# Optimization experiments

Measured on AMD Instinct MI355X. Metric: run time of the kernel, lower is better.

## Reference

```python
import jax, jax.numpy as jnp
import numpy as np

N_NODES = 100000
IN_CH = 65
HID_CH = 64
N_EDGES = 3200000


def setup_inputs() -> dict:
    key = jax.random.key(0)
    k1, k2, k3, k4, k5 = jax.random.split(key, 5)
    x = jax.random.normal(k1, (N_NODES, IN_CH), dtype=jnp.float32)
    edge_index = jax.random.randint(k2, (2, N_EDGES), 0, N_NODES, dtype=jnp.int64)
    edge_weight = jax.random.uniform(k3, (N_EDGES,), dtype=jnp.float32)
    # PyG GraphConv params: lin_rel (with bias) applied to aggregated neighbors,
    # lin_root (no bias) applied to self features.
    scale = 1.0 / np.sqrt(IN_CH)
    W_rel = jax.random.uniform(k4, (HID_CH, IN_CH), dtype=jnp.float32, minval=-scale, maxval=scale)
    b_rel = jnp.zeros((HID_CH,), dtype=jnp.float32)
    W_root = jax.random.uniform(k5, (HID_CH, IN_CH), dtype=jnp.float32, minval=-scale, maxval=scale)
    return {"x": x, "edge_index": edge_index, "edge_weight": edge_weight,
            "W_rel": W_rel, "b_rel": b_rel, "W_root": W_root}


def reference(x, edge_index, edge_weight, W_rel, b_rel, W_root):
    src = edge_index[0]  # source nodes (x_j in PyG message)
    dst = edge_index[1]  # target nodes (aggregation index)
    # gather neighbor features, weight by edge weight: [E, IN_CH]
    msgs = x[src] * edge_weight[:, None]
    # scatter-add to destination nodes: [N, IN_CH]
    aggr = jax.ops.segment_sum(msgs, dst, num_segments=N_NODES)
    # out = lin_rel(aggr) + lin_root(x)
    out = aggr @ W_rel.T + b_rel + x @ W_root.T
    return out
```

## Files before the change

kernel.cpp:

```cpp
#include <hip/hip_runtime.h>

#define IN_CH 65
#define HID 64
#define BN 64
#define NB 1563
#define CAP 2560
#define SCAP 2432
#define EPB 16384
#define TPS 1024
#define EPT (EPB / TPS)
#define WSTR 132

static inline size_t align16(size_t v) { return (v + 15) & ~(size_t)15; }

__device__ inline ushort f2bf(float f) {
    uint u = __float_as_uint(f);
    return (ushort)((u + 0x7FFF + ((u >> 16) & 1)) >> 16);
}
__device__ inline float bf2f(ushort h) { return __uint_as_float((uint)h << 16); }

__global__ __launch_bounds__(256) void k1(const float* __restrict__ x,
                                          const float* __restrict__ W_rel,
                                          const float* __restrict__ b_rel,
                                          const float* __restrict__ W_root,
                                          ushort* __restrict__ y16,
                                          float* __restrict__ out,
                                          int* __restrict__ cnt, int nBuckets,
                                          int nNodes) {
    __shared__ float xs[64 * IN_CH];
    __shared__ float ws[IN_CH * WSTR];
    const int tid = threadIdx.x;
    const int tx = tid & 15;
    const int ty = tid >> 4;
    const long nodeBase = (long)blockIdx.x * 64;
    const int nValid = min(64, nNodes - (int)nodeBase);
    const int nx = nValid * IN_CH;

    if (cnt && tid == 0 && blockIdx.x < (unsigned)nBuckets) cnt[blockIdx.x] = 0;

    for (int f = tid; f < HID * IN_CH; f += 256) {
        const int j = f / IN_CH, c = f - j * IN_CH;
        ws[c * WSTR + j] = W_rel[f];
    }
    for (int f = tid; f < HID * IN_CH; f += 256) {
        const int j = f / IN_CH, c = f - j * IN_CH;
        ws[c * WSTR + HID + j] = W_root[f];
    }
    const float* xsrc = x + nodeBase * IN_CH;
    for (int i = tid; i < 64 * IN_CH; i += 256) xs[i] = (i < nx) ? xsrc[i] : 0.f;
    __syncthreads();

    float acc[4][8];
#pragma unroll
    for (int i = 0; i < 4; ++i)
#pragma unroll
        for (int j = 0; j < 8; ++j) acc[i][j] = 0.f;

    const int r0 = ty * 4;
    const int c0 = tx * 8;
    for (int k = 0; k < IN_CH; ++k) {
        float aa[4] = {xs[(r0 + 0) * IN_CH + k], xs[(r0 + 1) * IN_CH + k],
                       xs[(r0 + 2) * IN_CH + k], xs[(r0 + 3) * IN_CH + k]};
        float4 b0 = *(const float4*)&ws[k * WSTR + c0];
        float4 b1 = *(const float4*)&ws[k * WSTR + c0 + 4];
        float bb[8] = {b0.x, b0.y, b0.z, b0.w, b1.x, b1.y, b1.z, b1.w};
#pragma unroll
        for (int i = 0; i < 4; ++i)
#pragma unroll
            for (int j = 0; j < 8; ++j) acc[i][j] += aa[i] * bb[j];
    }

    if (c0 >= HID) {
        const int h0 = c0 - HID;
        float4 bb0 = *(const float4*)&b_rel[h0];
        float4 bb1 = *(const float4*)&b_rel[h0 + 4];
        float bv[8] = {bb0.x, bb0.y, bb0.z, bb0.w, bb1.x, bb1.y, bb1.z, bb1.w};
#pragma unroll
        for (int i = 0; i < 4; ++i)
#pragma unroll
            for (int j = 0; j < 8; ++j) acc[i][j] += bv[j];
    }

#pragma unroll
    for (int i = 0; i < 4; ++i) {
        const long node = nodeBase + r0 + i;
        if (node >= nNodes) break;
        if (c0 < HID) {
            uint4 pk;
            pk.x = (uint)f2bf(acc[i][0]) | ((uint)f2bf(acc[i][1]) << 16);
            pk.y = (uint)f2bf(acc[i][2]) | ((uint)f2bf(acc[i][3]) << 16);
            pk.z = (uint)f2bf(acc[i][4]) | ((uint)f2bf(acc[i][5]) << 16);
            pk.w = (uint)f2bf(acc[i][6]) | ((uint)f2bf(acc[i][7]) << 16);
            *(uint4*)&y16[node * HID + c0] = pk;
        } else {
            float* dst = out + node * HID + (c0 - HID);
            *(float4*)(dst + 0) = make_float4(acc[i][0], acc[i][1], acc[i][2], acc[i][3]);
            *(float4*)(dst + 4) = make_float4(acc[i][4], acc[i][5], acc[i][6], acc[i][7]);
        }
    }
}

__global__ __launch_bounds__(TPS) void scatterB(const int* __restrict__ ei,
                                                const float* __restrict__ ew,
                                                int* __restrict__ cnt,
                                                int2* __restrict__ pairs, int E) {
    __shared__ int lhist[NB];
    __shared__ int lbase[NB];
    const int tid = threadIdx.x;
    const long e0 = (long)blockIdx.x * EPB;
    const int n = (int)min((long)EPB, (long)E - e0);

    for (int i = tid; i < NB; i += TPS) lhist[i] = 0;
    __syncthreads();

    int dstv[EPT], srcv[EPT];
    float wv[EPT];
#pragma unroll
    for (int k = 0; k < EPT; ++k) {
        const int i = tid + k * TPS;
        const bool valid = i < n;
        dstv[k] = valid ? ei[(long)E + e0 + i] : 0;
        srcv[k] = valid ? ei[e0 + i] : 0;
        wv[k]   = valid ? ew[e0 + i] : 0.f;
        if (valid) atomicAdd(&lhist[dstv[k] >> 6], 1);
    }
    __syncthreads();

    for (int i = tid; i < NB; i += TPS) {
        const int c = lhist[i];
        lbase[i] = c ? atomicAdd(&cnt[i], c) : 0;
        lhist[i] = 0;
    }
    __syncthreads();

#pragma unroll
    for (int k = 0; k < EPT; ++k) {
        const int i = tid + k * TPS;
        if (i < n) {
            const int b = dstv[k] >> 6;
            const int p = lbase[b] + atomicAdd(&lhist[b], 1);
            if (p < CAP)
                pairs[(size_t)b * CAP + p] =
                    make_int2((srcv[k] << 7) | ((dstv[k] & (BN - 1)) << 25),
                              __float_as_int(wv[k]));
        }
    }
}

__global__ __launch_bounds__(512) void aggregateS16(const int2* __restrict__ pairs,
                                                    const int* __restrict__ cnt,
                                                    const ushort* __restrict__ y16,
                                                    float* __restrict__ out, int N) {
    __shared__ int2 sorted[SCAP];
    __shared__ int sH[BN];
    __shared__ int soff[BN + 1];
    __shared__ int scur[BN];
    const int tid = threadIdx.x;
    const int lane = tid & 63;
    const int wv = tid >> 6;
    const int half = lane >> 5;
    const uint lane4 = (lane & 31) * 4;
    const int b = blockIdx.x;

    if (tid < BN) { sH[tid] = 0; scur[tid] = 0; }
    __syncthreads();

    const int m = min(cnt[b], CAP);
    const int2* pb = pairs + (size_t)b * CAP;

    int2 pv[5];
#pragma unroll
    for (int kk = 0; kk < 5; ++kk) {
        const int i = tid + kk * 512;
        if (i < m) {
            pv[kk] = pb[i];
            atomicAdd(&sH[(uint)pv[kk].x >> 25], 1);
        }
    }
    __syncthreads();

    for (int off = 1; off < BN; off <<= 1) {
        int v = 0;
        if (tid < BN) {
            v = sH[tid];
            if (tid >= off) v += sH[tid - off];
        }
        __syncthreads();
        if (tid < BN) sH[tid] = v;
        __syncthreads();
    }
    if (tid < BN) soff[tid + 1] = sH[tid];
    if (tid == 0) soff[0] = 0;
    __syncthreads();

#pragma unroll
    for (int kk = 0; kk < 5; ++kk) {
        const int i = tid + kk * 512;
        if (i < m) {
            const int d = (uint)pv[kk].x >> 25;
            const int slot = soff[d] + atomicAdd(&scur[d], 1);
            if (slot < SCAP) sorted[slot] = make_int2(pv[kk].x & 0x00FFFF80, pv[kk].y);
        }
    }
    __syncthreads();

    const char* yb = (const char*)y16;
    const long nodeBase = (long)b * BN;
    for (int nl = wv; nl < BN; nl += 8) {
        const long node = nodeBase + nl;
        if (node >= N) break;
        const int kbeg = min(soff[nl], SCAP);
        const int kend = min(soff[nl + 1], SCAP);
        float2* o = (float2*)(out + node * HID) + (lane & 31);
        const float2 cur = *o;
        float ax = 0.f, ay = 0.f;
        int k = kbeg + half;
        for (; k + 14 < kend; k += 16) {
            int2 pp[8];
#pragma unroll
            for (int j = 0; j < 8; ++j) pp[j] = sorted[k + 2 * j];
            uint qq[8];
#pragma unroll
            for (int j = 0; j < 8; ++j)
                qq[j] = *(const uint*)(yb + (uint)pp[j].x + lane4);
#pragma unroll
            for (int j = 0; j < 8; ++j) {
                const float w = __int_as_float(pp[j].y);
                ax += w * __uint_as_float(qq[j] << 16);
                ay += w * __uint_as_float(qq[j] & 0xFFFF0000u);
            }
        }
        for (; k + 6 < kend; k += 8) {
            const int2 p0 = sorted[k],     p1 = sorted[k + 2];
            const int2 p2 = sorted[k + 4], p3 = sorted[k + 6];
            const uint q0 = *(const uint*)(yb + (uint)p0.x + lane4);
            const uint q1 = *(const uint*)(yb + (uint)p1.x + lane4);
            const uint q2 = *(const uint*)(yb + (uint)p2.x + lane4);
            const uint q3 = *(const uint*)(yb + (uint)p3.x + lane4);
            const float w0 = __int_as_float(p0.y), w1 = __int_as_float(p1.y);
            const float w2 = __int_as_float(p2.y), w3 = __int_as_float(p3.y);
            ax += w0 * __uint_as_float(q0 << 16);
            ay += w0 * __uint_as_float(q0 & 0xFFFF0000u);
            ax += w1 * __uint_as_float(q1 << 16);
            ay += w1 * __uint_as_float(q1 & 0xFFFF0000u);
            ax += w2 * __uint_as_float(q2 << 16);
            ay += w2 * __uint_as_float(q2 & 0xFFFF0000u);
            ax += w3 * __uint_as_float(q3 << 16);
            ay += w3 * __uint_as_float(q3 & 0xFFFF0000u);
        }
        for (; k < kend; k += 2) {
            const int2 p = sorted[k];
            const uint q = *(const uint*)(yb + (uint)p.x + lane4);
            const float w = __int_as_float(p.y);
            ax += w * __uint_as_float(q << 16);
            ay += w * __uint_as_float(q & 0xFFFF0000u);
        }
        ax += __shfl_xor(ax, 32);
        ay += __shfl_xor(ay, 32);
        if (half == 0) {
            *o = make_float2(cur.x + ax, cur.y + ay);
        }
    }
}

__global__ __launch_bounds__(256) void k2_atomic16(const int* __restrict__ ei,
                                                   const float* __restrict__ ew,
                                                   const ushort* __restrict__ y16,
                                                   float* __restrict__ out, int E) {
    const long t = (long)blockIdx.x * 256 + threadIdx.x;
    const long e = t >> 4;
    const int r = (int)(t & 15);
    if (e >= E) return;
    const int src = ei[e];
    const int dst = ei[(long)E + e];
    const float w = ew[e];
    const uint2 q = ((const uint2*)y16)[(size_t)src * 16 + r];
    float* o = out + (size_t)dst * HID + r * 4;
    unsafeAtomicAdd(o + 0, w * __uint_as_float(q.x << 16));
    unsafeAtomicAdd(o + 1, w * __uint_as_float(q.x & 0xFFFF0000u));
    unsafeAtomicAdd(o + 2, w * __uint_as_float(q.y << 16));
    unsafeAtomicAdd(o + 3, w * __uint_as_float(q.y & 0xFFFF0000u));
}

extern "C" void kernel_launch(void* const* d_in, const int* in_sizes, int n_in,
                              void* d_out, int out_size, void* d_ws, size_t ws_size,
                              hipStream_t stream) {
    const float* x      = (const float*)d_in[0];
    const int*   ei     = (const int*)d_in[1];
    const float* ew     = (const float*)d_in[2];
    const float* W_rel  = (const float*)d_in[3];
    const float* b_rel  = (const float*)d_in[4];
    const float* W_root = (const float*)d_in[5];
    float* out = (float*)d_out;

    const int N = in_sizes[0] / IN_CH;
    const int E = in_sizes[2];

    char* base = (char*)d_ws;
    const size_t oY     = 0;
    const size_t oPairs = align16((size_t)N * HID * 2);
    const size_t oCnt   = oPairs + align16((size_t)NB * CAP * 8);
    const size_t need   = oCnt + (size_t)NB * 4;

    ushort* y16 = (ushort*)(base + oY);
    const int nb1 = (N + 63) / 64;

    const bool fits = (ws_size >= need) && (N <= (1 << 17)) &&
                      ((size_t)NB * BN >= (size_t)N) && ((long)E <= (long)N * 33) &&
                      (nb1 >= NB);

    if (fits) {
        int2* pairs = (int2*)(base + oPairs);
        int*  cnt   = (int*)(base + oCnt);

        k1<<<nb1, 256, 0, stream>>>(x, W_rel, b_rel, W_root, y16, out, cnt, NB, N);
        scatterB<<<(E + EPB - 1) / EPB, TPS, 0, stream>>>(ei, ew, cnt, pairs, E);
        aggregateS16<<<NB, 512, 0, stream>>>(pairs, cnt, y16, out, N);
    } else {
        k1<<<nb1, 256, 0, stream>>>(x, W_rel, b_rel, W_root, y16, out,
                                    (int*)nullptr, 0, N);
        const long thr2 = (long)E * 16;
        k2_atomic16<<<(int)((thr2 + 255) / 256), 256, 0, stream>>>(ei, ew, y16, out, E);
    }
}
```

Measured before the change: 243.9 us.

## Move root linear into aggregation kernel and retile first GEMM to 128 nodes

The first kernel now computes only the W_rel projection (bf16 y) over 128-node tiles with a transposed x tile in shared memory. The root projection plus bias is computed inside the aggregation kernel from x for its 64-node bucket and staged in shared memory, so the final write is a single store per output instead of a write in k1 followed by a read-modify-write. The intent is to cut out the fp32 out round trip through HBM. The cost is that aggregation blocks must load x and W_root and do extra FMAs, and shared memory use per block grows.

```diff
diff --git a/kernel.cpp b/kernel.cpp
--- a/kernel.cpp
+++ b/kernel.cpp
@@ -17,37 +17,35 @@
     uint u = __float_as_uint(f);
     return (ushort)((u + 0x7FFF + ((u >> 16) & 1)) >> 16);
 }
-__device__ inline float bf2f(ushort h) { return __uint_as_float((uint)h << 16); }
-
-__global__ __launch_bounds__(256) void k1(const float* __restrict__ x,
-                                          const float* __restrict__ W_rel,
-                                          const float* __restrict__ b_rel,
-                                          const float* __restrict__ W_root,
-                                          ushort* __restrict__ y16,
-                                          float* __restrict__ out,
-                                          int* __restrict__ cnt, int nBuckets,
-                                          int nNodes) {
-    __shared__ float xs[64 * IN_CH];
-    __shared__ float ws[IN_CH * WSTR];
+
+__global__ __launch_bounds__(256) void k1y(const float* __restrict__ x,
+                                           const float* __restrict__ W_rel,
+                                           ushort* __restrict__ y16,
+                                           int* __restrict__ cnt, int nBuckets,
+                                           int nNodes) {
+    __shared__ float xsT[65 * 132];
+    __shared__ float ws[65 * 68];
     const int tid = threadIdx.x;
-    const int tx = tid & 15;
-    const int ty = tid >> 4;
-    const long nodeBase = (long)blockIdx.x * 64;
-    const int nValid = min(64, nNodes - (int)nodeBase);
-    const int nx = nValid * IN_CH;
-
-    if (cnt && tid == 0 && blockIdx.x < (unsigned)nBuckets) cnt[blockIdx.x] = 0;
+    const int tx = tid & 7;
+    const int ty = tid >> 3;
+    const long nodeBase = (long)blockIdx.x * 128;
+    const int nValid = (int)min((long)128, (long)nNodes - nodeBase);
+
+    if (cnt) {
+        const int c2 = blockIdx.x * 2;
+        if (tid == 0 && c2 < nBuckets) cnt[c2] = 0;
+        if (tid == 1 && c2 + 1 < nBuckets) cnt[c2 + 1] = 0;
+    }
 
     for (int f = tid; f < HID * IN_CH; f += 256) {
         const int j = f / IN_CH, c = f - j * IN_CH;
-        ws[c * WSTR + j] = W_rel[f];
-    }
-    for (int f = tid; f < HID * IN_CH; f += 256) {
-        const int j = f / IN_CH, c = f - j * IN_CH;
-        ws[c * WSTR + HID + j] = W_root[f];
+        ws[c * 68 + j] = W_rel[f];
     }
     const float* xsrc = x + nodeBase * IN_CH;
-    for (int i = tid; i < 64 * IN_CH; i += 256) xs[i] = (i < nx) ? xsrc[i] : 0.f;
+    for (int f = tid; f < 128 * IN_CH; f += 256) {
+        const int node = f / IN_CH, k = f - node * IN_CH;
+        xsT[k * 132 + node] = (node < nValid) ? xsrc[f] : 0.f;
+    }
     __syncthreads();
 
     float acc[4][8];
@@ -59,44 +57,27 @@
     const int r0 = ty * 4;
     const int c0 = tx * 8;
     for (int k = 0; k < IN_CH; ++k) {
-        float aa[4] = {xs[(r0 + 0) * IN_CH + k], xs[(r0 + 1) * IN_CH + k],
-                       xs[(r0 + 2) * IN_CH + k], xs[(r0 + 3) * IN_CH + k]};
-        float4 b0 = *(const float4*)&ws[k * WSTR + c0];
-        float4 b1 = *(const float4*)&ws[k * WSTR + c0 + 4];
-        float bb[8] = {b0.x, b0.y, b0.z, b0.w, b1.x, b1.y, b1.z, b1.w};
+        const float4 a4 = *(const float4*)&xsT[k * 132 + r0];
+        const float4 b0 = *(const float4*)&ws[k * 68 + c0];
+        const float4 b1 = *(const float4*)&ws[k * 68 + c0 + 4];
+        const float aa[4] = {a4.x, a4.y, a4.z, a4.w};
+        const float bb[8] = {b0.x, b0.y, b0.z, b0.w, b1.x, b1.y, b1.z, b1.w};
 #pragma unroll
         for (int i = 0; i < 4; ++i)
 #pragma unroll
             for (int j = 0; j < 8; ++j) acc[i][j] += aa[i] * bb[j];
-    }
-
-    if (c0 >= HID) {
-        const int h0 = c0 - HID;
-        float4 bb0 = *(const float4*)&b_rel[h0];
-        float4 bb1 = *(const float4*)&b_rel[h0 + 4];
-        float bv[8] = {bb0.x, bb0.y, bb0.z, bb0.w, bb1.x, bb1.y, bb1.z, bb1.w};
-#pragma unroll
-        for (int i = 0; i < 4; ++i)
-#pragma unroll
-            for (int j = 0; j < 8; ++j) acc[i][j] += bv[j];
     }
 
 #pragma unroll
     for (int i = 0; i < 4; ++i) {
         const long node = nodeBase + r0 + i;
         if (node >= nNodes) break;
-        if (c0 < HID) {
-            uint4 pk;
-            pk.x = (uint)f2bf(acc[i][0]) | ((uint)f2bf(acc[i][1]) << 16);
-            pk.y = (uint)f2bf(acc[i][2]) | ((uint)f2bf(acc[i][3]) << 16);
-            pk.z = (uint)f2bf(acc[i][4]) | ((uint)f2bf(acc[i][5]) << 16);
-            pk.w = (uint)f2bf(acc[i][6]) | ((uint)f2bf(acc[i][7]) << 16);
-            *(uint4*)&y16[node * HID + c0] = pk;
-        } else {
-            float* dst = out + node * HID + (c0 - HID);
-            *(float4*)(dst + 0) = make_float4(acc[i][0], acc[i][1], acc[i][2], acc[i][3]);
-            *(float4*)(dst + 4) = make_float4(acc[i][4], acc[i][5], acc[i][6], acc[i][7]);
-        }
+        uint4 pk;
+        pk.x = (uint)f2bf(acc[i][0]) | ((uint)f2bf(acc[i][1]) << 16);
+        pk.y = (uint)f2bf(acc[i][2]) | ((uint)f2bf(acc[i][3]) << 16);
+        pk.z = (uint)f2bf(acc[i][4]) | ((uint)f2bf(acc[i][5]) << 16);
+        pk.w = (uint)f2bf(acc[i][6]) | ((uint)f2bf(acc[i][7]) << 16);
+        *(uint4*)&y16[node * HID + c0] = pk;
     }
 }
 
@@ -150,20 +131,25 @@
 __global__ __launch_bounds__(512) void aggregateS16(const int2* __restrict__ pairs,
                                                     const int* __restrict__ cnt,
                                                     const ushort* __restrict__ y16,
+                                                    const float* __restrict__ x,
+                                                    const float* __restrict__ W_root,
+                                                    const float* __restrict__ b_rel,
                                                     float* __restrict__ out, int N) {
-    __shared__ int2 sorted[SCAP];
-    __shared__ int sH[BN];
-    __shared__ int soff[BN + 1];
-    __shared__ int scur[BN];
+    __shared__ __align__(16) char smem[19456 + 17408 + 4 * (BN + BN + 1 + BN) + 16];
+    float* xs       = (float*)smem;
+    int2*  sorted   = (int2*)smem;
+    float* rootBuf  = (float*)(smem + 19456);
+    int*   sH       = (int*)(smem + 36864);
+    int*   soff     = sH + BN;
+    int*   scur     = soff + BN + 1;
+
     const int tid = threadIdx.x;
     const int lane = tid & 63;
-    const int wv = tid >> 6;
+    const int wvid = tid >> 6;
     const int half = lane >> 5;
     const uint lane4 = (lane & 31) * 4;
     const int b = blockIdx.x;
-
-    if (tid < BN) { sH[tid] = 0; scur[tid] = 0; }
-    __syncthreads();
+    const long nodeBase = (long)b * BN;
 
     const int m = min(cnt[b], CAP);
     const int2* pb = pairs + (size_t)b * CAP;
@@ -172,10 +158,39 @@
 #pragma unroll
     for (int kk = 0; kk < 5; ++kk) {
         const int i = tid + kk * 512;
-        if (i < m) {
-            pv[kk] = pb[i];
-            atomicAdd(&sH[(uint)pv[kk].x >> 25], 1);
-        }
+        if (i < m) pv[kk] = pb[i];
+    }
+
+    const int nValid = (int)min((long)BN, (long)N - nodeBase);
+    const int nx = nValid * IN_CH;
+    const float* xsrc = x + nodeBase * IN_CH;
+    for (int i = tid; i < BN * IN_CH; i += 512) xs[i] = (i < nx) ? xsrc[i] : 0.f;
+
+    if (tid < BN) { sH[tid] = 0; scur[tid] = 0; }
+    __syncthreads();
+
+#pragma unroll
+    for (int kk = 0; kk < 5; ++kk) {
+        const int i = tid + kk * 512;
+        if (i < m) atomicAdd(&sH[(uint)pv[kk].x >> 25], 1);
+    }
+
+    {
+        const int wvu = __builtin_amdgcn_readfirstlane(wvid);
+        const int c0 = wvu * 8;
+        float racc[8];
+#pragma unroll
+        for (int j = 0; j < 8; ++j) racc[j] = b_rel[c0 + j];
+        const float* xrow = xs + lane * IN_CH;
+        const float* wb = W_root + (size_t)c0 * IN_CH;
+        for (int k = 0; k < IN_CH; ++k) {
+            const float xv = xrow[k];
+#pragma unroll
+            for (int j = 0; j < 8; ++j) racc[j] += xv * wb[j * IN_CH + k];
+        }
+        float* rb = rootBuf + lane * 68 + c0;
+        *(float4*)(rb + 0) = make_float4(racc[0], racc[1], racc[2], racc[3]);
+        *(float4*)(rb + 4) = make_float4(racc[4], racc[5], racc[6], racc[7]);
     }
     __syncthreads();
 
@@ -205,14 +220,11 @@
     __syncthreads();
 
     const char* yb = (const char*)y16;
-    const long nodeBase = (long)b * BN;
-    for (int nl = wv; nl < BN; nl += 8) {
+    for (int nl = wvid; nl < BN; nl += 8) {
         const long node = nodeBase + nl;
         if (node >= N) break;
         const int kbeg = min(soff[nl], SCAP);
         const int kend = min(soff[nl + 1], SCAP);
-        float2* o = (float2*)(out + node * HID) + (lane & 31);
-        const float2 cur = *o;
         float ax = 0.f, ay = 0.f;
         int k = kbeg + half;
         for (; k + 14 < kend; k += 16) {
@@ -258,7 +270,87 @@
         ax += __shfl_xor(ax, 32);
         ay += __shfl_xor(ay, 32);
         if (half == 0) {
-            *o = make_float2(cur.x + ax, cur.y + ay);
+            const float2 rb = *(const float2*)&rootBuf[nl * 68 + (lane & 31) * 2];
+            float2* o = (float2*)(out + node * HID) + (lane & 31);
+            *o = make_float2(rb.x + ax, rb.y + ay);
+        }
+    }
+}
+
+__global__ __launch_bounds__(256) void k1_full(const float* __restrict__ x,
+                                               const float* __restrict__ W_rel,
+                                               const float* __restrict__ b_rel,
+                                               const float* __restrict__ W_root,
+                                               ushort* __restrict__ y16,
+                                               float* __restrict__ out,
+                                               int nNodes) {
+    __shared__ float xs[64 * IN_CH];
+    __shared__ float ws[IN_CH * WSTR];
+    const int tid = threadIdx.x;
+    const int tx = tid & 15;
+    const int ty = tid >> 4;
+    const long nodeBase = (long)blockIdx.x * 64;
+    const int nValid = min(64, nNodes - (int)nodeBase);
+    const int nx = nValid * IN_CH;
+
+    for (int f = tid; f < HID * IN_CH; f += 256) {
+        const int j = f / IN_CH, c = f - j * IN_CH;
+        ws[c * WSTR + j] = W_rel[f];
+    }
+    for (int f = tid; f < HID * IN_CH; f += 256) {
+        const int j = f / IN_CH, c = f - j * IN_CH;
+        ws[c * WSTR + HID + j] = W_root[f];
+    }
+    const float* xsrc = x + nodeBase * IN_CH;
+    for (int i = tid; i < 64 * IN_CH; i += 256) xs[i] = (i < nx) ? xsrc[i] : 0.f;
+    __syncthreads();
+
+    float acc[4][8];
+#pragma unroll
+    for (int i = 0; i < 4; ++i)
+#pragma unroll
+        for (int j = 0; j < 8; ++j) acc[i][j] = 0.f;
+
+    const int r0 = ty * 4;
+    const int c0 = tx * 8;
+    for (int k = 0; k < IN_CH; ++k) {
+        float aa[4] = {xs[(r0 + 0) * IN_CH + k], xs[(r0 + 1) * IN_CH + k],
+                       xs[(r0 + 2) * IN_CH + k], xs[(r0 + 3) * IN_CH + k]};
+        float4 b0 = *(const float4*)&ws[k * WSTR + c0];
+        float4 b1 = *(const float4*)&ws[k * WSTR + c0 + 4];
+        float bb[8] = {b0.x, b0.y, b0.z, b0.w, b1.x, b1.y, b1.z, b1.w};
+#pragma unroll
+        for (int i = 0; i < 4; ++i)
+#pragma unroll
+            for (int j = 0; j < 8; ++j) acc[i][j] += aa[i] * bb[j];
+    }
+
+    if (c0 >= HID) {
+        const int h0 = c0 - HID;
+        float4 bb0 = *(const float4*)&b_rel[h0];
+        float4 bb1 = *(const float4*)&b_rel[h0 + 4];
+        float bv[8] = {bb0.x, bb0.y, bb0.z, bb0.w, bb1.x, bb1.y, bb1.z, bb1.w};
+#pragma unroll
+        for (int i = 0; i < 4; ++i)
+#pragma unroll
+            for (int j = 0; j < 8; ++j) acc[i][j] += bv[j];
+    }
+
+#pragma unroll
+    for (int i = 0; i < 4; ++i) {
+        const long node = nodeBase + r0 + i;
+        if (node >= nNodes) break;
+        if (c0 < HID) {
+            uint4 pk;
+            pk.x = (uint)f2bf(acc[i][0]) | ((uint)f2bf(acc[i][1]) << 16);
+            pk.y = (uint)f2bf(acc[i][2]) | ((uint)f2bf(acc[i][3]) << 16);
+            pk.z = (uint)f2bf(acc[i][4]) | ((uint)f2bf(acc[i][5]) << 16);
+            pk.w = (uint)f2bf(acc[i][6]) | ((uint)f2bf(acc[i][7]) << 16);
+            *(uint4*)&y16[node * HID + c0] = pk;
+        } else {
+            float* dst = out + node * HID + (c0 - HID);
+            *(float4*)(dst + 0) = make_float4(acc[i][0], acc[i][1], acc[i][2], acc[i][3]);
+            *(float4*)(dst + 4) = make_float4(acc[i][4], acc[i][5], acc[i][6], acc[i][7]);
         }
     }
 }
@@ -303,22 +395,22 @@
     const size_t need   = oCnt + (size_t)NB * 4;
 
     ushort* y16 = (ushort*)(base + oY);
-    const int nb1 = (N + 63) / 64;
+    const int nb1 = (N + 127) / 128;
 
     const bool fits = (ws_size >= need) && (N <= (1 << 17)) &&
                       ((size_t)NB * BN >= (size_t)N) && ((long)E <= (long)N * 33) &&
-                      (nb1 >= NB);
+                      (2 * nb1 >= NB);
 
     if (fits) {
         int2* pairs = (int2*)(base + oPairs);
         int*  cnt   = (int*)(base + oCnt);
 
-        k1<<<nb1, 256, 0, stream>>>(x, W_rel, b_rel, W_root, y16, out, cnt, NB, N);
+        k1y<<<nb1, 256, 0, stream>>>(x, W_rel, y16, cnt, NB, N);
         scatterB<<<(E + EPB - 1) / EPB, TPS, 0, stream>>>(ei, ew, cnt, pairs, E);
-        aggregateS16<<<NB, 512, 0, stream>>>(pairs, cnt, y16, out, N);
+        aggregateS16<<<NB, 512, 0, stream>>>(pairs, cnt, y16, x, W_root, b_rel, out, N);
     } else {
-        k1<<<nb1, 256, 0, stream>>>(x, W_rel, b_rel, W_root, y16, out,
-                                    (int*)nullptr, 0, N);
+        const int nbf = (N + 63) / 64;
+        k1_full<<<nbf, 256, 0, stream>>>(x, W_rel, b_rel, W_root, y16, out, N);
         const long thr2 = (long)E * 16;
         k2_atomic16<<<(int)((thr2 + 255) / 256), 256, 0, stream>>>(ei, ew, y16, out, E);
     }
```

Result: faster. 234.9 us (-3.7%).
